# Kernel tuning notes

Measured on AMD Instinct MI355X. Metric: run time of the kernel, lower is better.

Reference implementation:

```python
import jax, jax.numpy as jnp
import numpy as np

D_MODEL = 256
D_STATE = 64
D_CONV = 4
EXPAND = 2
HEADDIM = 64
D_INNER = EXPAND * D_MODEL            # 512
NHEADS = D_INNER // HEADDIM           # 8
CONV_DIM = D_INNER + 2 * D_STATE      # 640 (ngroups=1)
BATCH = 8
SEQ = 4096


def setup_inputs() -> dict:
    key = jax.random.key(0)
    ks = jax.random.split(key, 6)
    x = jax.random.normal(ks[0], (BATCH, SEQ, D_MODEL), jnp.float32)
    d_in_proj = 2 * D_INNER + 2 * D_STATE + NHEADS  # 1160
    W_in = jax.random.normal(ks[1], (d_in_proj, D_MODEL), jnp.float32) / np.sqrt(D_MODEL)
    conv_w = jax.random.normal(ks[2], (CONV_DIM, D_CONV), jnp.float32) / np.sqrt(D_CONV)
    conv_b = jnp.zeros((CONV_DIM,), jnp.float32)
    # dt_bias = inverse-softplus of dt sampled log-uniform in [1e-3, 0.1] (mamba_ssm init)
    dt = jnp.exp(jax.random.uniform(ks[3], (NHEADS,), jnp.float32, np.log(1e-3), np.log(0.1)))
    dt_bias = dt + jnp.log(-jnp.expm1(-dt))
    A_log = jnp.log(jax.random.uniform(ks[4], (NHEADS,), jnp.float32, 1.0, 16.0))
    Dp = jnp.ones((NHEADS,), jnp.float32)
    gnorm_w = jnp.ones((D_INNER,), jnp.float32)
    norm_w = jnp.ones((D_MODEL,), jnp.float32)
    W_out = jax.random.normal(ks[5], (D_MODEL, D_INNER), jnp.float32) / np.sqrt(D_INNER)
    return {"x": x, "W_in": W_in, "conv_w": conv_w, "conv_b": conv_b,
            "dt_bias": dt_bias, "A_log": A_log, "Dp": Dp,
            "gnorm_w": gnorm_w, "norm_w": norm_w, "W_out": W_out}


def _rmsnorm(x, w, eps):
    return x * jax.lax.rsqrt(jnp.mean(x * x, axis=-1, keepdims=True) + eps) * w


def reference(x, W_in, conv_w, conv_b, dt_bias, A_log, Dp, gnorm_w, norm_w, W_out):
    Bsz, L, _ = x.shape
    # pre-norm (torch nn.RMSNorm eps=None -> finfo eps)
    xn = _rmsnorm(x, norm_w, jnp.finfo(x.dtype).eps)
    zxbcdt = jnp.einsum('bld,ed->ble', xn, W_in)            # (B,L,1160)
    z = zxbcdt[..., :D_INNER]                               # gate (B,L,512)
    xBC = zxbcdt[..., D_INNER:D_INNER + CONV_DIM]           # (B,L,640)
    dt = zxbcdt[..., -NHEADS:]                              # (B,L,8)
    # causal depthwise conv1d + silu
    xpad = jnp.pad(xBC, ((0, 0), (D_CONV - 1, 0), (0, 0)))
    conv = sum(xpad[:, k:k + L, :] * conv_w[:, k] for k in range(D_CONV)) + conv_b
    xBC = jax.nn.silu(conv)
    xs = xBC[..., :D_INNER].reshape(Bsz, L, NHEADS, HEADDIM)  # (B,L,H,P)
    Bm = xBC[..., D_INNER:D_INNER + D_STATE]                  # (B,L,N)
    Cm = xBC[..., D_INNER + D_STATE:]                         # (B,L,N)
    dt = jax.nn.softplus(dt + dt_bias)                        # (B,L,H)
    dA = jnp.exp(dt * (-jnp.exp(A_log)))                      # (B,L,H)

    def step(state, inp):
        dA_t, dt_t, B_t, C_t, x_t = inp  # (B,H) (B,H) (B,N) (B,N) (B,H,P)
        state = state * dA_t[:, :, None, None] \
            + (dt_t[:, :, None] * x_t)[..., None] * B_t[:, None, None, :]
        y = jnp.einsum('bhpn,bn->bhp', state, C_t)
        return state, y

    init = jnp.zeros((Bsz, NHEADS, HEADDIM, D_STATE), x.dtype)
    tm = lambda a: jnp.moveaxis(a, 1, 0)  # time-major for scan
    _, ys = jax.lax.scan(step, init, (tm(dA), tm(dt), tm(Bm), tm(Cm), tm(xs)))
    y = jnp.moveaxis(ys, 0, 1) + Dp[None, None, :, None] * xs  # skip D term
    y = y.reshape(Bsz, L, D_INNER)
    # gated RMSNorm (norm_before_gate=False): rmsnorm(y * silu(z))
    y = _rmsnorm(y * jax.nn.silu(z), gnorm_w, 1e-5)
    return x + jnp.einsum('ble,de->bld', y, W_out)
```

## Files before the change

### kernel.cpp

```cpp
#include <hip/hip_runtime.h>
#include <math.h>

#define BATCH   8
#define SEQ     4096
#define DMODEL  256
#define DINNER  512
#define DSTATE  64
#define NHEADS  8
#define HEADDIM 64
#define CONVDIM 640
#define DPROJ   1160
#define NROWS   (BATCH*SEQ)
#define CHUNK   64
#define NCHUNK  (SEQ/CHUNK)
#define NPAD    1280
#define LSTR    72

typedef short bf16x8 __attribute__((ext_vector_type(8)));
typedef short short8v __attribute__((ext_vector_type(8)));
typedef float f32x4 __attribute__((ext_vector_type(4)));

__device__ short g_xn[(size_t)NROWS * DMODEL];
__device__ short g_zxb[(size_t)NROWS * DPROJ];
__device__ short g_xbc[(size_t)NROWS * CONVDIM];
__device__ float g_dt[(size_t)NROWS * NHEADS];
__device__ short g_yzn[(size_t)NROWS * DINNER];
__device__ short g_lstate[(size_t)BATCH * NHEADS * NCHUNK * HEADDIM * DSTATE];
__device__ float g_decayC[BATCH * NHEADS * NCHUNK];
__device__ short g_Winb[(size_t)NPAD * DMODEL];
__device__ short g_Woutb[(size_t)DMODEL * DINNER];

__device__ __forceinline__ short f2bf(float f) {
    unsigned u = __float_as_uint(f);
    u += 0x7fff + ((u >> 16) & 1);
    return (short)(u >> 16);
}
__device__ __forceinline__ float bf2f(short s) {
    return __uint_as_float(((unsigned)(unsigned short)s) << 16);
}

__device__ __forceinline__ void stage16(const void* gsrc, void* ldst) {
    __builtin_amdgcn_global_load_lds(
        (const __attribute__((address_space(1))) void*)gsrc,
        (__attribute__((address_space(3))) void*)ldst, 16, 0, 0);
}

__global__ __launch_bounds__(256) void convert_bf16_kernel(const float* __restrict__ src,
                                                           short* __restrict__ dst,
                                                           int n_valid, int n_total) {
    const int i = blockIdx.x * 256 + threadIdx.x;
    if (i < n_total) dst[i] = (i < n_valid) ? f2bf(src[i]) : (short)0;
}

__global__ __launch_bounds__(256) void rmsnorm_dt_kernel(const float* __restrict__ x,
                                                         const float* __restrict__ w,
                                                         const float* __restrict__ W_in,
                                                         short* __restrict__ xn,
                                                         float* __restrict__ dt) {
    const int row  = blockIdx.x * 4 + (threadIdx.x >> 6);
    const int lane = threadIdx.x & 63;
    const float4 v = *(const float4*)(x + (size_t)row * DMODEL + lane * 4);
    float ss = v.x * v.x + v.y * v.y + v.z * v.z + v.w * v.w;
#pragma unroll
    for (int off = 1; off < 64; off <<= 1) ss += __shfl_xor(ss, off);
    const float rs = rsqrtf(ss * (1.0f / DMODEL) + 1.1920929e-7f);
    const float4 wv = *(const float4*)(w + lane * 4);
    const float4 xn4 = make_float4(v.x * rs * wv.x, v.y * rs * wv.y,
                                   v.z * rs * wv.z, v.w * rs * wv.w);
    short4 o;
    o.x = f2bf(xn4.x); o.y = f2bf(xn4.y); o.z = f2bf(xn4.z); o.w = f2bf(xn4.w);
    *(short4*)(xn + (size_t)row * DMODEL + lane * 4) = o;
#pragma unroll
    for (int h = 0; h < NHEADS; ++h) {
        const float4 ww = *(const float4*)(W_in + (size_t)(DPROJ - NHEADS + h) * DMODEL + lane * 4);
        float p = xn4.x * ww.x + xn4.y * ww.y + xn4.z * ww.z + xn4.w * ww.w;
#pragma unroll
        for (int off = 1; off < 64; off <<= 1) p += __shfl_xor(p, off);
        if (lane == 0) dt[(size_t)row * NHEADS + h] = p;
    }
}

template <bool RES, typename OUT>
__global__ __launch_bounds__(256) void gemm_bf16_nt(const short* __restrict__ A,
                                                    const short* __restrict__ B,
                                                    const float* __restrict__ R,
                                                    OUT* __restrict__ C,
                                                    int NX, int M, int N, int K) {
    const int L   = blockIdx.x;
    const int xcd = L & 7;
    const int r   = L >> 3;
    const int mstrips_per_xcd = (M / 128) >> 3;
    const int mblk = xcd * mstrips_per_xcd + r / NX;
    const int nblk = r % NX;
    const int m0 = mblk * 128, n0 = nblk * 128;

    __shared__ __align__(16) short Asl[128 * 64];
    __shared__ __align__(16) short Bsl[128 * 64];
    const int tid  = threadIdx.x;
    const int lane = tid & 63;
    const int wid  = tid >> 6;
    const int wrow = (wid >> 1) * 64, wcol = (wid & 1) * 64;

    f32x4 acc[4][4];
#pragma unroll
    for (int m = 0; m < 4; ++m)
#pragma unroll
        for (int n = 0; n < 4; ++n) acc[m][n] = (f32x4)0.f;

    const int wbase = (tid & 0xC0) * 8;

    for (int k0 = 0; k0 < K; k0 += 64) {
#pragma unroll
        for (int rr = 0; rr < 4; ++rr) {
            const int idx = rr * 256 + tid;
            const int row = idx >> 3;
            const int cs  = idx & 7;
            const int ko  = (cs ^ (row & 7)) * 8;
            const int r6  = row & 63;
            const int brow = (row & 64) + (((r6 & 15) << 2) | (r6 >> 4));
            stage16(A + (size_t)(m0 + row) * K + k0 + ko, Asl + rr * 2048 + wbase);
            stage16(B + (size_t)(n0 + brow) * K + k0 + ko, Bsl + rr * 2048 + wbase);
        }
        __syncthreads();
#pragma unroll
        for (int ks = 0; ks < 2; ++ks) {
            bf16x8 af[4], bfr[4];
#pragma unroll
            for (int m = 0; m < 4; ++m) {
                const int arow = wrow + m * 16 + (lane & 15);
                const int ch = (ks * 4 + (lane >> 4)) ^ (arow & 7);
                af[m] = *(const bf16x8*)(Asl + arow * 64 + ch * 8);
            }
#pragma unroll
            for (int n = 0; n < 4; ++n) {
                const int brw = wcol + n * 16 + (lane & 15);
                const int ch = (ks * 4 + (lane >> 4)) ^ (brw & 7);
                bfr[n] = *(const bf16x8*)(Bsl + brw * 64 + ch * 8);
            }
#pragma unroll
            for (int m = 0; m < 4; ++m)
#pragma unroll
                for (int n = 0; n < 4; ++n)
                    acc[m][n] = __builtin_amdgcn_mfma_f32_16x16x32_bf16(af[m], bfr[n], acc[m][n], 0, 0, 0);
        }
        __syncthreads();
    }

    const int r0 = (lane >> 4) * 4;
    const int gcol = n0 + wcol + (lane & 15) * 4;
#pragma unroll
    for (int m = 0; m < 4; ++m) {
        const int grow = m0 + wrow + m * 16 + r0;
        if (gcol < N) {
#pragma unroll
            for (int reg = 0; reg < 4; ++reg) {
                if constexpr (sizeof(OUT) == 2) {
                    short4 o;
                    o.x = f2bf(acc[m][0][reg]); o.y = f2bf(acc[m][1][reg]);
                    o.z = f2bf(acc[m][2][reg]); o.w = f2bf(acc[m][3][reg]);
                    *(short4*)(C + (size_t)(grow + reg) * N + gcol) = o;
                } else {
                    f32x4 v;
                    v[0] = acc[m][0][reg]; v[1] = acc[m][1][reg];
                    v[2] = acc[m][2][reg]; v[3] = acc[m][3][reg];
                    if (RES) v += *(const f32x4*)(R + (size_t)(grow + reg) * N + gcol);
                    *(f32x4*)(C + (size_t)(grow + reg) * N + gcol) = v;
                }
            }
        }
    }
}

__global__ __launch_bounds__(256) void conv_silu_kernel(const short* __restrict__ zxb,
                                                        const float* __restrict__ cw,
                                                        const float* __restrict__ cb,
                                                        short* __restrict__ xbc) {
    const int idx = blockIdx.x * 256 + threadIdx.x;
    const int c8  = (idx % 80) * 8;
    const int bl0 = (idx / 80) * 4;
    const int l0  = bl0 & (SEQ - 1);
    const short* src = zxb + (size_t)bl0 * DPROJ + DINNER + c8;

    float4 w4[8];
    float bias[8];
#pragma unroll
    for (int j = 0; j < 8; ++j) w4[j] = *(const float4*)(cw + (c8 + j) * 4);
    {
        const float4 b0 = *(const float4*)(cb + c8);
        const float4 b1 = *(const float4*)(cb + c8 + 4);
        bias[0] = b0.x; bias[1] = b0.y; bias[2] = b0.z; bias[3] = b0.w;
        bias[4] = b1.x; bias[5] = b1.y; bias[6] = b1.z; bias[7] = b1.w;
    }

    bf16x8 rowv[7];
#pragma unroll
    for (int m = 0; m < 7; ++m) {
        if (l0 + m - 3 >= 0)
            rowv[m] = *(const bf16x8*)(src + (ptrdiff_t)(m - 3) * DPROJ);
        else
            rowv[m] = (bf16x8)0;
    }

#pragma unroll
    for (int r = 0; r < 4; ++r) {
        float acc[8];
#pragma unroll
        for (int j = 0; j < 8; ++j) acc[j] = bias[j];
#pragma unroll
        for (int k = 0; k < 4; ++k) {
            const bf16x8 tap = rowv[r + k];
#pragma unroll
            for (int j = 0; j < 8; ++j)
                acc[j] = fmaf(bf2f(tap[j]), ((const float*)&w4[j])[k], acc[j]);
        }
        short8v o;
#pragma unroll
        for (int j = 0; j < 8; ++j) {
            const float s = acc[j];
            o[j] = f2bf(s / (1.f + __expf(-s)));
        }
        *(short8v*)(xbc + (size_t)(bl0 + r) * CONVDIM + c8) = o;
    }
}

__global__ __launch_bounds__(256) void chunk_state_mfma(const float* __restrict__ dt,
                                                        const short* __restrict__ xbc,
                                                        const float* __restrict__ dt_bias,
                                                        const float* __restrict__ A_log,
                                                        short* __restrict__ lstate,
                                                        float* __restrict__ decayC) {
    const int bhc = blockIdx.x;
    const int c = bhc & (NCHUNK - 1), bh = bhc >> 6, h = bh & (NHEADS - 1), b = bh >> 3;
    const int tid = threadIdx.x, lane = tid & 63, wid = tid >> 6;
    __shared__ short XT[64 * LSTR];
    __shared__ short BT[64 * LSTR];
    __shared__ float wsh[CHUNK];
    const size_t row0 = (size_t)b * SEQ + (size_t)c * CHUNK;

    const float aneg  = -__expf(A_log[h]);
    const float dbias = dt_bias[h];
    if (tid < 64) {
        const float draw = dt[(row0 + tid) * NHEADS + h] + dbias;
        const float dtv  = (draw > 20.f) ? draw : log1pf(__expf(draw));
        float cum = aneg * dtv;
#pragma unroll
        for (int off = 1; off < 64; off <<= 1) {
            const float nv = __shfl_up(cum, off);
            if (lane >= off) cum += nv;
        }
        const float total = __shfl(cum, 63);
        wsh[tid] = __expf(total - cum) * dtv;
        if (tid == 63) decayC[bhc] = __expf(cum);
    }
    __syncthreads();

#pragma unroll
    for (int r = 0; r < 4; ++r) {
        const int idx  = tid + r * 256;
        const int trow = idx >> 4;
        const int q    = idx & 15;
        const int c4   = q * 4;
        const short* rp = xbc + (row0 + trow) * CONVDIM;
        const short4 xv = *(const short4*)(rp + h * 64 + c4);
        const short4 bv = *(const short4*)(rp + DINNER + c4);
        const float w = wsh[trow];
        XT[(c4 + 0) * LSTR + trow] = xv.x;
        XT[(c4 + 1) * LSTR + trow] = xv.y;
        XT[(c4 + 2) * LSTR + trow] = xv.z;
        XT[(c4 + 3) * LSTR + trow] = xv.w;
        BT[(0 * 16 + q) * LSTR + trow] = f2bf(bf2f(bv.x) * w);
        BT[(1 * 16 + q) * LSTR + trow] = f2bf(bf2f(bv.y) * w);
        BT[(2 * 16 + q) * LSTR + trow] = f2bf(bf2f(bv.z) * w);
        BT[(3 * 16 + q) * LSTR + trow] = f2bf(bf2f(bv.w) * w);
    }
    __syncthreads();

    f32x4 acc[4];
#pragma unroll
    for (int n = 0; n < 4; ++n) acc[n] = (f32x4)0.f;
#pragma unroll
    for (int ks = 0; ks < 2; ++ks) {
        const bf16x8 af = *(const bf16x8*)(XT + (wid * 16 + (lane & 15)) * LSTR + ks * 32 + (lane >> 4) * 8);
#pragma unroll
        for (int n = 0; n < 4; ++n) {
            const bf16x8 bfv = *(const bf16x8*)(BT + (n * 16 + (lane & 15)) * LSTR + ks * 32 + (lane >> 4) * 8);
            acc[n] = __builtin_amdgcn_mfma_f32_16x16x32_bf16(af, bfv, acc[n], 0, 0, 0);
        }
    }
    short* lp = lstate + ((size_t)bhc << 12);
    const int ncol = (lane & 15) * 4;
#pragma unroll
    for (int reg = 0; reg < 4; ++reg) {
        const int p = wid * 16 + (lane >> 4) * 4 + reg;
        short4 o;
        o.x = f2bf(acc[0][reg]); o.y = f2bf(acc[1][reg]);
        o.z = f2bf(acc[2][reg]); o.w = f2bf(acc[3][reg]);
        *(short4*)(lp + p * 64 + ncol) = o;
    }
}

__global__ __launch_bounds__(256) void state_prefix_kernel(short* __restrict__ lstate,
                                                           const float* __restrict__ decayC) {
    const int idx = blockIdx.x * 256 + threadIdx.x;
    const int bh = idx >> 12;
    const int pn = idx & 4095;
    float S = 0.f;
    for (int c = 0; c < NCHUNK; ++c) {
        short* ptr = lstate + (((size_t)bh * NCHUNK + c) << 12) + pn;
        const float l = bf2f(*ptr);
        *ptr = f2bf(S);
        S = fmaf(S, decayC[bh * NCHUNK + c], l);
    }
}

__global__ __launch_bounds__(256) void chunk_scan_mfma(const float* __restrict__ dt,
                                                       short* __restrict__ xbc,
                                                       const float* __restrict__ dt_bias,
                                                       const float* __restrict__ A_log,
                                                       const float* __restrict__ Dp,
                                                       const short* __restrict__ lstate) {
    const int bhc = blockIdx.x;
    const int c = bhc & (NCHUNK - 1), bh = bhc >> 6, h = bh & (NHEADS - 1), b = bh >> 3;
    const int tid = threadIdx.x, lane = tid & 63, wid = tid >> 6;
    __shared__ short Bs[64 * LSTR];
    __shared__ short Cs[64 * LSTR];
    __shared__ short XT[64 * LSTR];
    __shared__ short SP[64 * LSTR];
    __shared__ short Ms[64 * LSTR];
    __shared__ float cums[CHUNK];
    __shared__ float dtss[CHUNK];
    const size_t row0 = (size_t)b * SEQ + (size_t)c * CHUNK;

#pragma unroll
    for (int r = 0; r < 4; ++r) {
        const int idx  = tid + r * 256;
        const int trow = idx >> 4;
        const int q    = idx & 15;
        const int c4   = q * 4;
        const short* rp = xbc + (row0 + trow) * CONVDIM;
        const short4 xv = *(const short4*)(rp + h * 64 + c4);
        *(short4*)(Bs + trow * LSTR + c4) = *(const short4*)(rp + DINNER + c4);
        *(short4*)(Cs + trow * LSTR + c4) = *(const short4*)(rp + DINNER + DSTATE + c4);
        XT[(0 * 16 + q) * LSTR + trow] = xv.x;
        XT[(1 * 16 + q) * LSTR + trow] = xv.y;
        XT[(2 * 16 + q) * LSTR + trow] = xv.z;
        XT[(3 * 16 + q) * LSTR + trow] = xv.w;
    }
#pragma unroll
    for (int r = 0; r < 4; ++r) {
        const int idx = tid + r * 256;
        const int p = idx >> 4, n4 = (idx & 15) * 4;
        const int pslot = ((p & 3) << 4) | (p >> 2);
        *(short4*)(SP + pslot * LSTR + n4) =
            *(const short4*)(lstate + ((size_t)bhc << 12) + p * 64 + n4);
    }
    const float aneg  = -__expf(A_log[h]);
    const float dbias = dt_bias[h];
    if (tid < 64) {
        const float draw = dt[(row0 + tid) * NHEADS + h] + dbias;
        const float dtv  = (draw > 20.f) ? draw : log1pf(__expf(draw));
        float cum = aneg * dtv;
#pragma unroll
        for (int off = 1; off < 64; off <<= 1) {
            const float nv = __shfl_up(cum, off);
            if (lane >= off) cum += nv;
        }
        cums[tid] = cum;
        dtss[tid] = dtv;
    }
    __syncthreads();

    f32x4 accG[4];
#pragma unroll
    for (int tf = 0; tf < 4; ++tf) accG[tf] = (f32x4)0.f;
#pragma unroll
    for (int ks = 0; ks < 2; ++ks) {
        const bf16x8 af = *(const bf16x8*)(Cs + (wid * 16 + (lane & 15)) * LSTR + ks * 32 + (lane >> 4) * 8);
#pragma unroll
        for (int tf = 0; tf < 4; ++tf) {
            const bf16x8 bfv = *(const bf16x8*)(Bs + (tf * 16 + (lane & 15)) * LSTR + ks * 32 + (lane >> 4) * 8);
            accG[tf] = __builtin_amdgcn_mfma_f32_16x16x32_bf16(af, bfv, accG[tf], 0, 0, 0);
        }
    }
    const int srow0 = wid * 16 + (lane >> 4) * 4;
#pragma unroll
    for (int tf = 0; tf < 4; ++tf) {
        const int t = tf * 16 + (lane & 15);
        const float ct  = cums[t];
        const float dtt = dtss[t];
#pragma unroll
        for (int reg = 0; reg < 4; ++reg) {
            const int s = srow0 + reg;
            const float m = (t <= s) ? accG[tf][reg] * __expf(cums[s] - ct) * dtt : 0.f;
            Ms[s * LSTR + t] = f2bf(m);
        }
    }
    __syncthreads();

    f32x4 acc1[4], acc2[4];
#pragma unroll
    for (int pf = 0; pf < 4; ++pf) { acc1[pf] = (f32x4)0.f; acc2[pf] = (f32x4)0.f; }
#pragma unroll
    for (int ks = 0; ks < 2; ++ks) {
        const bf16x8 am = *(const bf16x8*)(Ms + (wid * 16 + (lane & 15)) * LSTR + ks * 32 + (lane >> 4) * 8);
        const bf16x8 ac = *(const bf16x8*)(Cs + (wid * 16 + (lane & 15)) * LSTR + ks * 32 + (lane >> 4) * 8);
#pragma unroll
        for (int pf = 0; pf < 4; ++pf) {
            const bf16x8 bx = *(const bf16x8*)(XT + (pf * 16 + (lane & 15)) * LSTR + ks * 32 + (lane >> 4) * 8);
            const bf16x8 bs = *(const bf16x8*)(SP + (pf * 16 + (lane & 15)) * LSTR + ks * 32 + (lane >> 4) * 8);
            acc1[pf] = __builtin_amdgcn_mfma_f32_16x16x32_bf16(am, bx, acc1[pf], 0, 0, 0);
            acc2[pf] = __builtin_amdgcn_mfma_f32_16x16x32_bf16(ac, bs, acc2[pf], 0, 0, 0);
        }
    }
    const float dpv = Dp[h];
    float es[4];
#pragma unroll
    for (int reg = 0; reg < 4; ++reg) es[reg] = __expf(cums[srow0 + reg]);
    const int j = lane & 15;
#pragma unroll
    for (int reg = 0; reg < 4; ++reg) {
        const int s = srow0 + reg;
        short4 o;
#pragma unroll
        for (int pf = 0; pf < 4; ++pf) {
            const float xv = bf2f(XT[(pf * 16 + j) * LSTR + s]);
            const float yv = acc1[pf][reg] + es[reg] * acc2[pf][reg] + dpv * xv;
            ((short*)&o)[pf] = f2bf(yv);
        }
        *(short4*)(xbc + (row0 + s) * CONVDIM + h * 64 + j * 4) = o;
    }
}

__global__ __launch_bounds__(256) void gate_norm_kernel(const short* __restrict__ xbc,
                                                        const short* __restrict__ zxb,
                                                        const float* __restrict__ gw,
                                                        short* __restrict__ yzn) {
    const int row  = blockIdx.x * 4 + (threadIdx.x >> 6);
    const int lane = threadIdx.x & 63;
    const bf16x8 yv8 = *(const bf16x8*)(xbc + (size_t)row * CONVDIM + lane * 8);
    const bf16x8 zv  = *(const bf16x8*)(zxb + (size_t)row * DPROJ + lane * 8);
    float v[8];
#pragma unroll
    for (int i = 0; i < 8; ++i) {
        const float z = bf2f(zv[i]);
        v[i] = bf2f(yv8[i]) * z / (1.f + __expf(-z));
    }
    float ss = 0.f;
#pragma unroll
    for (int i = 0; i < 8; ++i) ss += v[i] * v[i];
#pragma unroll
    for (int off = 1; off < 64; off <<= 1) ss += __shfl_xor(ss, off);
    const float rs = rsqrtf(ss * (1.0f / DINNER) + 1e-5f);
    const float* g = gw + lane * 8;
    short8v o;
#pragma unroll
    for (int i = 0; i < 8; ++i) o[i] = f2bf(v[i] * rs * g[i]);
    *(short8v*)(yzn + (size_t)row * DINNER + lane * 8) = o;
}

extern "C" void kernel_launch(void* const* d_in, const int* in_sizes, int n_in,
                              void* d_out, int out_size, void* d_ws, size_t ws_size,
                              hipStream_t stream) {
    (void)in_sizes; (void)n_in; (void)out_size; (void)d_ws; (void)ws_size;
    const float* x      = (const float*)d_in[0];
    const float* W_in   = (const float*)d_in[1];
    const float* conv_w = (const float*)d_in[2];
    const float* conv_b = (const float*)d_in[3];
    const float* dt_b   = (const float*)d_in[4];
    const float* A_log  = (const float*)d_in[5];
    const float* Dp     = (const float*)d_in[6];
    const float* g_w    = (const float*)d_in[7];
    const float* n_w    = (const float*)d_in[8];
    const float* W_out  = (const float*)d_in[9];
    float* out = (float*)d_out;

    short *xn, *zxb, *xbc, *yzn, *winb, *woutb, *lst;
    float *dtv, *dcy;
    hipGetSymbolAddress((void**)&xn,    HIP_SYMBOL(g_xn));
    hipGetSymbolAddress((void**)&zxb,   HIP_SYMBOL(g_zxb));
    hipGetSymbolAddress((void**)&xbc,   HIP_SYMBOL(g_xbc));
    hipGetSymbolAddress((void**)&dtv,   HIP_SYMBOL(g_dt));
    hipGetSymbolAddress((void**)&yzn,   HIP_SYMBOL(g_yzn));
    hipGetSymbolAddress((void**)&lst,   HIP_SYMBOL(g_lstate));
    hipGetSymbolAddress((void**)&dcy,   HIP_SYMBOL(g_decayC));
    hipGetSymbolAddress((void**)&winb,  HIP_SYMBOL(g_Winb));
    hipGetSymbolAddress((void**)&woutb, HIP_SYMBOL(g_Woutb));

    convert_bf16_kernel<<<(NPAD * DMODEL) / 256, 256, 0, stream>>>(
        W_in, winb, DPROJ * DMODEL, NPAD * DMODEL);
    convert_bf16_kernel<<<(DMODEL * DINNER) / 256, 256, 0, stream>>>(
        W_out, woutb, DMODEL * DINNER, DMODEL * DINNER);

    rmsnorm_dt_kernel<<<NROWS / 4, 256, 0, stream>>>(x, n_w, W_in, xn, dtv);

    gemm_bf16_nt<false, short><<<(NPAD / 128) * (NROWS / 128), 256, 0, stream>>>(
        xn, winb, nullptr, zxb, NPAD / 128, NROWS, DPROJ, DMODEL);

    conv_silu_kernel<<<(NROWS / 4 * 80) / 256, 256, 0, stream>>>(zxb, conv_w, conv_b, xbc);

    chunk_state_mfma<<<BATCH * NHEADS * NCHUNK, 256, 0, stream>>>(dtv, xbc, dt_b, A_log, lst, dcy);
    state_prefix_kernel<<<(BATCH * NHEADS * HEADDIM * DSTATE) / 256, 256, 0, stream>>>(lst, dcy);
    chunk_scan_mfma<<<BATCH * NHEADS * NCHUNK, 256, 0, stream>>>(dtv, xbc, dt_b, A_log, Dp, lst);

    gate_norm_kernel<<<NROWS / 4, 256, 0, stream>>>(xbc, zxb, g_w, yzn);

    gemm_bf16_nt<true, float><<<(DMODEL / 128) * (NROWS / 128), 256, 0, stream>>>(
        yzn, woutb, x, out, DMODEL / 128, NROWS, DMODEL, DINNER);
}
```

Before: 193.8 us.

## Fuse gated RMSNorm into chunk scan and out-projection epilogue

```diff
diff --git a/kernel.cpp b/kernel.cpp
--- a/kernel.cpp
+++ b/kernel.cpp
@@ -24,7 +24,7 @@
 __device__ short g_zxb[(size_t)NROWS * DPROJ];
 __device__ short g_xbc[(size_t)NROWS * CONVDIM];
 __device__ float g_dt[(size_t)NROWS * NHEADS];
-__device__ short g_yzn[(size_t)NROWS * DINNER];
+__device__ float g_rowss[(size_t)NROWS * NHEADS];
 __device__ short g_lstate[(size_t)BATCH * NHEADS * NCHUNK * HEADDIM * DSTATE];
 __device__ float g_decayC[BATCH * NHEADS * NCHUNK];
 __device__ short g_Winb[(size_t)NPAD * DMODEL];
@@ -50,6 +50,13 @@
                                                            int n_valid, int n_total) {
     const int i = blockIdx.x * 256 + threadIdx.x;
     if (i < n_total) dst[i] = (i < n_valid) ? f2bf(src[i]) : (short)0;
+}
+
+__global__ __launch_bounds__(256) void convert_wout_kernel(const float* __restrict__ src,
+                                                           const float* __restrict__ gw,
+                                                           short* __restrict__ dst) {
+    const int i = blockIdx.x * 256 + threadIdx.x;
+    if (i < DMODEL * DINNER) dst[i] = f2bf(src[i] * gw[i % DINNER]);
 }
 
 __global__ __launch_bounds__(256) void rmsnorm_dt_kernel(const float* __restrict__ x,
@@ -84,8 +91,9 @@
 __global__ __launch_bounds__(256) void gemm_bf16_nt(const short* __restrict__ A,
                                                     const short* __restrict__ B,
                                                     const float* __restrict__ R,
+                                                    const float* __restrict__ RS,
                                                     OUT* __restrict__ C,
-                                                    int NX, int M, int N, int K) {
+                                                    int NX, int M, int N, int K, int LDA) {
     const int L   = blockIdx.x;
     const int xcd = L & 7;
     const int r   = L >> 3;
@@ -118,7 +126,7 @@
             const int ko  = (cs ^ (row & 7)) * 8;
             const int r6  = row & 63;
             const int brow = (row & 64) + (((r6 & 15) << 2) | (r6 >> 4));
-            stage16(A + (size_t)(m0 + row) * K + k0 + ko, Asl + rr * 2048 + wbase);
+            stage16(A + (size_t)(m0 + row) * LDA + k0 + ko, Asl + rr * 2048 + wbase);
             stage16(B + (size_t)(n0 + brow) * K + k0 + ko, Bsl + rr * 2048 + wbase);
         }
         __syncthreads();
@@ -163,7 +171,16 @@
                     f32x4 v;
                     v[0] = acc[m][0][reg]; v[1] = acc[m][1][reg];
                     v[2] = acc[m][2][reg]; v[3] = acc[m][3][reg];
-                    if (RES) v += *(const f32x4*)(R + (size_t)(grow + reg) * N + gcol);
+                    if (RES) {
+                        const float* rp = RS + (size_t)(grow + reg) * NHEADS;
+                        const f32x4 s0 = *(const f32x4*)rp;
+                        const f32x4 s1 = *(const f32x4*)(rp + 4);
+                        const float sum = s0[0] + s0[1] + s0[2] + s0[3] +
+                                          s1[0] + s1[1] + s1[2] + s1[3];
+                        const float rsn = rsqrtf(sum * (1.0f / DINNER) + 1e-5f);
+                        v *= rsn;
+                        v += *(const f32x4*)(R + (size_t)(grow + reg) * N + gcol);
+                    }
                     *(f32x4*)(C + (size_t)(grow + reg) * N + gcol) = v;
                 }
             }
@@ -177,7 +194,7 @@
                                                         short* __restrict__ xbc) {
     const int idx = blockIdx.x * 256 + threadIdx.x;
     const int c8  = (idx % 80) * 8;
-    const int bl0 = (idx / 80) * 4;
+    const int bl0 = (idx / 80) * 8;
     const int l0  = bl0 & (SEQ - 1);
     const short* src = zxb + (size_t)bl0 * DPROJ + DINNER + c8;
 
@@ -192,9 +209,9 @@
         bias[4] = b1.x; bias[5] = b1.y; bias[6] = b1.z; bias[7] = b1.w;
     }
 
-    bf16x8 rowv[7];
-#pragma unroll
-    for (int m = 0; m < 7; ++m) {
+    bf16x8 rowv[11];
+#pragma unroll
+    for (int m = 0; m < 11; ++m) {
         if (l0 + m - 3 >= 0)
             rowv[m] = *(const bf16x8*)(src + (ptrdiff_t)(m - 3) * DPROJ);
         else
@@ -202,7 +219,7 @@
     }
 
 #pragma unroll
-    for (int r = 0; r < 4; ++r) {
+    for (int r = 0; r < 8; ++r) {
         float acc[8];
 #pragma unroll
         for (int j = 0; j < 8; ++j) acc[j] = bias[j];
@@ -315,6 +332,8 @@
 
 __global__ __launch_bounds__(256) void chunk_scan_mfma(const float* __restrict__ dt,
                                                        short* __restrict__ xbc,
+                                                       const short* __restrict__ zxb,
+                                                       float* __restrict__ rowss,
                                                        const float* __restrict__ dt_bias,
                                                        const float* __restrict__ A_log,
                                                        const float* __restrict__ Dp,
@@ -420,42 +439,25 @@
 #pragma unroll
     for (int reg = 0; reg < 4; ++reg) {
         const int s = srow0 + reg;
+        const short4 z4 = *(const short4*)(zxb + (row0 + s) * DPROJ + h * 64 + j * 4);
         short4 o;
+        float ssq = 0.f;
 #pragma unroll
         for (int pf = 0; pf < 4; ++pf) {
             const float xv = bf2f(XT[(pf * 16 + j) * LSTR + s]);
             const float yv = acc1[pf][reg] + es[reg] * acc2[pf][reg] + dpv * xv;
-            ((short*)&o)[pf] = f2bf(yv);
+            const float zf = bf2f(((const short*)&z4)[pf]);
+            const float v  = yv * zf / (1.f + __expf(-zf));
+            ((short*)&o)[pf] = f2bf(v);
+            ssq = fmaf(v, v, ssq);
         }
         *(short4*)(xbc + (row0 + s) * CONVDIM + h * 64 + j * 4) = o;
-    }
-}
-
-__global__ __launch_bounds__(256) void gate_norm_kernel(const short* __restrict__ xbc,
-                                                        const short* __restrict__ zxb,
-                                                        const float* __restrict__ gw,
-                                                        short* __restrict__ yzn) {
-    const int row  = blockIdx.x * 4 + (threadIdx.x >> 6);
-    const int lane = threadIdx.x & 63;
-    const bf16x8 yv8 = *(const bf16x8*)(xbc + (size_t)row * CONVDIM + lane * 8);
-    const bf16x8 zv  = *(const bf16x8*)(zxb + (size_t)row * DPROJ + lane * 8);
-    float v[8];
-#pragma unroll
-    for (int i = 0; i < 8; ++i) {
-        const float z = bf2f(zv[i]);
-        v[i] = bf2f(yv8[i]) * z / (1.f + __expf(-z));
-    }
-    float ss = 0.f;
-#pragma unroll
-    for (int i = 0; i < 8; ++i) ss += v[i] * v[i];
-#pragma unroll
-    for (int off = 1; off < 64; off <<= 1) ss += __shfl_xor(ss, off);
-    const float rs = rsqrtf(ss * (1.0f / DINNER) + 1e-5f);
-    const float* g = gw + lane * 8;
-    short8v o;
-#pragma unroll
-    for (int i = 0; i < 8; ++i) o[i] = f2bf(v[i] * rs * g[i]);
-    *(short8v*)(yzn + (size_t)row * DINNER + lane * 8) = o;
+        ssq += __shfl_xor(ssq, 1);
+        ssq += __shfl_xor(ssq, 2);
+        ssq += __shfl_xor(ssq, 4);
+        ssq += __shfl_xor(ssq, 8);
+        if (j == 0) rowss[(row0 + s) * NHEADS + h] = ssq;
+    }
 }
 
 extern "C" void kernel_launch(void* const* d_in, const int* in_sizes, int n_in,
@@ -474,13 +476,13 @@
     const float* W_out  = (const float*)d_in[9];
     float* out = (float*)d_out;
 
-    short *xn, *zxb, *xbc, *yzn, *winb, *woutb, *lst;
-    float *dtv, *dcy;
+    short *xn, *zxb, *xbc, *winb, *woutb, *lst;
+    float *dtv, *dcy, *rss;
     hipGetSymbolAddress((void**)&xn,    HIP_SYMBOL(g_xn));
     hipGetSymbolAddress((void**)&zxb,   HIP_SYMBOL(g_zxb));
     hipGetSymbolAddress((void**)&xbc,   HIP_SYMBOL(g_xbc));
     hipGetSymbolAddress((void**)&dtv,   HIP_SYMBOL(g_dt));
-    hipGetSymbolAddress((void**)&yzn,   HIP_SYMBOL(g_yzn));
+    hipGetSymbolAddress((void**)&rss,   HIP_SYMBOL(g_rowss));
     hipGetSymbolAddress((void**)&lst,   HIP_SYMBOL(g_lstate));
     hipGetSymbolAddress((void**)&dcy,   HIP_SYMBOL(g_decayC));
     hipGetSymbolAddress((void**)&winb,  HIP_SYMBOL(g_Winb));
@@ -488,22 +490,20 @@
 
     convert_bf16_kernel<<<(NPAD * DMODEL) / 256, 256, 0, stream>>>(
         W_in, winb, DPROJ * DMODEL, NPAD * DMODEL);
-    convert_bf16_kernel<<<(DMODEL * DINNER) / 256, 256, 0, stream>>>(
-        W_out, woutb, DMODEL * DINNER, DMODEL * DINNER);
+    convert_wout_kernel<<<(DMODEL * DINNER) / 256, 256, 0, stream>>>(W_out, g_w, woutb);
 
     rmsnorm_dt_kernel<<<NROWS / 4, 256, 0, stream>>>(x, n_w, W_in, xn, dtv);
 
     gemm_bf16_nt<false, short><<<(NPAD / 128) * (NROWS / 128), 256, 0, stream>>>(
-        xn, winb, nullptr, zxb, NPAD / 128, NROWS, DPROJ, DMODEL);
-
-    conv_silu_kernel<<<(NROWS / 4 * 80) / 256, 256, 0, stream>>>(zxb, conv_w, conv_b, xbc);
+        xn, winb, nullptr, nullptr, zxb, NPAD / 128, NROWS, DPROJ, DMODEL, DMODEL);
+
+    conv_silu_kernel<<<(NROWS / 8 * 80) / 256, 256, 0, stream>>>(zxb, conv_w, conv_b, xbc);
 
     chunk_state_mfma<<<BATCH * NHEADS * NCHUNK, 256, 0, stream>>>(dtv, xbc, dt_b, A_log, lst, dcy);
     state_prefix_kernel<<<(BATCH * NHEADS * HEADDIM * DSTATE) / 256, 256, 0, stream>>>(lst, dcy);
-    chunk_scan_mfma<<<BATCH * NHEADS * NCHUNK, 256, 0, stream>>>(dtv, xbc, dt_b, A_log, Dp, lst);
-
-    gate_norm_kernel<<<NROWS / 4, 256, 0, stream>>>(xbc, zxb, g_w, yzn);
+    chunk_scan_mfma<<<BATCH * NHEADS * NCHUNK, 256, 0, stream>>>(
+        dtv, xbc, zxb, rss, dt_b, A_log, Dp, lst);
 
     gemm_bf16_nt<true, float><<<(DMODEL / 128) * (NROWS / 128), 256, 0, stream>>>(
-        yzn, woutb, x, out, DMODEL / 128, NROWS, DMODEL, DINNER);
-}
+        xbc, woutb, x, rss, out, DMODEL / 128, NROWS, DMODEL, DINNER, CONVDIM);
+}
```

Measured after the change: 188.4 us. 2.8% less time.
